# Kernel optimization log

Measured on AMD Instinct MI355X. Metric: run time of the kernel, lower is better.

## Reference

```python
import jax, jax.numpy as jnp
import numpy as np

N_NODES = 10000
N_EDGES = 160000
IN_DIM = 512
HID = 128
HEADS = 8
EMB = 256
NEG_SLOPE = 0.2  # PyG GATConv default


def setup_inputs() -> dict:
    key = jax.random.key(0)
    ks = jax.random.split(key, 12)
    x = jax.random.normal(ks[0], (N_NODES, IN_DIM), dtype=jnp.float32)
    edge_index = jax.random.randint(ks[1], (2, N_EDGES), 0, N_NODES, dtype=jnp.int64)
    s1 = 1.0 / np.sqrt(IN_DIM)
    s2 = 1.0 / np.sqrt(HEADS * HID)
    W1 = jax.random.normal(ks[2], (IN_DIM, HEADS * HID), dtype=jnp.float32) * s1
    a_src1 = jax.random.normal(ks[3], (HEADS, HID), dtype=jnp.float32) * s2
    a_dst1 = jax.random.normal(ks[4], (HEADS, HID), dtype=jnp.float32) * s2
    b1 = jnp.zeros((HEADS * HID,), dtype=jnp.float32)
    W2 = jax.random.normal(ks[5], (HEADS * HID, EMB), dtype=jnp.float32) * s2
    a_src2 = jax.random.normal(ks[6], (1, EMB), dtype=jnp.float32) * (1.0 / np.sqrt(EMB))
    a_dst2 = jax.random.normal(ks[7], (1, EMB), dtype=jnp.float32) * (1.0 / np.sqrt(EMB))
    b2 = jnp.zeros((EMB,), dtype=jnp.float32)
    return {"x": x, "edge_index": edge_index, "W1": W1, "a_src1": a_src1,
            "a_dst1": a_dst1, "b1": b1, "W2": W2, "a_src2": a_src2,
            "a_dst2": a_dst2, "b2": b2}


def gat_layer(h_in, src, dst, W, a_src, a_dst, b, concat, num_nodes):
    """PyG-style GATConv (eval mode, self-loops already in src/dst)."""
    H, C = a_src.shape
    h = (h_in @ W).reshape(num_nodes, H, C)            # [N, H, C]
    alpha_src = jnp.einsum('nhc,hc->nh', h, a_src)      # [N, H]
    alpha_dst = jnp.einsum('nhc,hc->nh', h, a_dst)      # [N, H]
    e = jax.nn.leaky_relu(alpha_src[src] + alpha_dst[dst], NEG_SLOPE)  # [E, H]
    # segment softmax over incoming edges of each destination node
    m = jax.ops.segment_max(e, dst, num_segments=num_nodes)            # [N, H]
    ex = jnp.exp(e - m[dst])
    denom = jax.ops.segment_sum(ex, dst, num_segments=num_nodes)       # [N, H]
    alpha = ex / denom[dst]                                            # [E, H]
    out = jax.ops.segment_sum(h[src] * alpha[:, :, None], dst,
                              num_segments=num_nodes)                  # [N, H, C]
    out = out.reshape(num_nodes, H * C) if concat else out.mean(axis=1)
    return out + b


def reference(x, edge_index, W1, a_src1, a_dst1, b1, W2, a_src2, a_dst2, b2):
    N = x.shape[0]
    loops = jnp.arange(N, dtype=edge_index.dtype)
    src = jnp.concatenate([edge_index[0], loops])
    dst = jnp.concatenate([edge_index[1], loops])
    h = gat_layer(x, src, dst, W1, a_src1, a_dst1, b1, concat=True, num_nodes=N)
    h = jax.nn.elu(h)  # dropout inactive in eval mode
    out = gat_layer(h, src, dst, W2, a_src2, a_dst2, b2, concat=False, num_nodes=N)
    return out
```

## Files before the change

### kernel.cpp

```cpp
#include <hip/hip_runtime.h>
#include <hip/hip_bf16.h>

typedef __attribute__((ext_vector_type(8))) short short8;
typedef __attribute__((ext_vector_type(4))) float floatx4;
typedef __attribute__((ext_vector_type(4))) unsigned short ushort4v;
typedef __attribute__((ext_vector_type(8))) unsigned short ushort8v;
typedef __attribute__((ext_vector_type(2))) unsigned int uint2v;
typedef __attribute__((ext_vector_type(4))) unsigned int uint4v;

#define NN 10000
#define E0 160000
#define ETOT (E0 + NN)
#define IN_DIM 512
#define HID1 1024
#define EMB 256
#define MPAD 10112
#define NX (NN * IN_DIM)
#define NW1 (IN_DIM * HID1)
#define NW2 (HID1 * EMB)

__device__ __forceinline__ float bf2f(unsigned short u) {
    unsigned v = ((unsigned)u) << 16;
    float f;
    __builtin_memcpy(&f, &v, 4);
    return f;
}
__device__ __forceinline__ float bflo(unsigned v) {
    unsigned x = v << 16;
    float f; __builtin_memcpy(&f, &x, 4);
    return f;
}
__device__ __forceinline__ float bfhi(unsigned v) {
    unsigned x = v & 0xffff0000u;
    float f; __builtin_memcpy(&f, &x, 4);
    return f;
}
__device__ __forceinline__ unsigned short f2bf(float f) {
    unsigned u;
    __builtin_memcpy(&u, &f, 4);
    unsigned lsb = (u >> 16) & 1;
    u += 0x7fff + lsb;
    return (unsigned short)(u >> 16);
}
__device__ __forceinline__ float loadf(const void* p, size_t i, int isf32) {
    if (isf32) return ((const float*)p)[i];
    return bf2f(((const unsigned short*)p)[i]);
}
__device__ __forceinline__ float lrelu(float e) { return e > 0.f ? e : 0.2f * e; }

__global__ __launch_bounds__(256) void probezero_kernel(
    const int* __restrict__ ei32, const unsigned* __restrict__ xw,
    int* __restrict__ zbase, int zn, int* __restrict__ eflag, int* __restrict__ isf32)
{
    int b = blockIdx.x, t = threadIdx.x;
    int i = b * 256 + t;
    if (i < zn) zbase[i] = 0;
    if (b == 0) {
        int any = 0;
        #pragma unroll
        for (int k = 0; k < 64; ++k) {
            int idx = (t + k * 256) * 2 + 1;
            any |= ei32[idx];
        }
        __shared__ int sf;
        if (t == 0) sf = 0;
        __syncthreads();
        if (any) atomicOr(&sf, 1);
        __syncthreads();
        if (t == 0) *eflag = sf;
    } else if (b == 1) {
        __shared__ int cnt[256];
        int c = 0;
        #pragma unroll
        for (int j = 0; j < 16; ++j) {
            unsigned w = xw[t * 16 + j];
            int ex = (w >> 7) & 0xFF;
            if (ex >= 110 && ex <= 135) c++;
        }
        cnt[t] = c;
        __syncthreads();
        for (int off = 128; off > 0; off >>= 1) {
            if (t < off) cnt[t] += cnt[t + off];
            __syncthreads();
        }
        if (t == 0) *isf32 = (cnt[0] < 2048) ? 1 : 0;
    }
}

__device__ __forceinline__ int load_edge(const void* ei, long long idx, int m32) {
    if (m32) return ((const int*)ei)[idx];
    return (int)(((const long long*)ei)[idx]);
}

__global__ void count_kernel(const void* ei, const int* flag, int* counts) {
    int e = blockIdx.x * 256 + threadIdx.x;
    if (e < E0) {
        int m32 = (*flag != 0);
        int d = load_edge(ei, (long long)E0 + e, m32);
        if (d >= 0 && d < NN) atomicAdd(&counts[d], 1);
    }
}

__global__ __launch_bounds__(1024) void scan_kernel(const int* counts, int* offsets, int* cursor) {
    __shared__ int wsum[16];
    int t = threadIdx.x;
    int lane = t & 63, wv = t >> 6;
    int base = t * 10;
    int local[10];
    int s = 0;
    #pragma unroll
    for (int j = 0; j < 10; ++j) {
        int idx = base + j;
        int v = (idx < NN) ? (counts[idx] + 1) : 0;
        local[j] = v; s += v;
    }
    int v = s;
    #pragma unroll
    for (int d = 1; d < 64; d <<= 1) {
        int o = __shfl_up(v, d, 64);
        if (lane >= d) v += o;
    }
    if (lane == 63) wsum[wv] = v;
    __syncthreads();
    if (t < 16) {
        int w = wsum[t];
        #pragma unroll
        for (int d = 1; d < 16; d <<= 1) {
            int o = __shfl_up(w, d, 16);
            if (t >= d) w += o;
        }
        wsum[t] = w;
    }
    __syncthreads();
    int woff = (wv == 0) ? 0 : wsum[wv - 1];
    int run = woff + v - s;
    #pragma unroll
    for (int j = 0; j < 10; ++j) {
        int idx = base + j;
        if (idx < NN) { offsets[idx] = run; cursor[idx] = run; run += local[j]; }
    }
    if (t == 1023) offsets[NN] = wsum[15];
}

__global__ void scatter_kernel(const void* ei, const int* flag, int* cursor, int* csr_src) {
    int e = blockIdx.x * 256 + threadIdx.x;
    if (e >= ETOT) return;
    int m32 = (*flag != 0);
    int s, d;
    if (e < E0) { s = load_edge(ei, e, m32); d = load_edge(ei, (long long)E0 + e, m32); }
    else { s = d = e - E0; }
    if (s < 0) s = 0; if (s >= NN) s = NN - 1;
    if (d < 0) d = 0; if (d >= NN) d = NN - 1;
    int pos = atomicAdd(&cursor[d], 1);
    if (pos >= 0 && pos < ETOT) csr_src[pos] = s;
}

__global__ void convall_kernel(const void* x, const void* W1, const void* W2,
                               unsigned short* xb, unsigned short* W1t, unsigned short* W2t,
                               const int* isf32)
{
    int i = blockIdx.x * 256 + threadIdx.x;
    int f = *isf32;
    if (i < NX) { xb[i] = f2bf(loadf(x, i, f)); return; }
    i -= NX;
    if (i < NW1) {
        int r = i / HID1, c = i % HID1;
        W1t[(size_t)c * IN_DIM + r] = f2bf(loadf(W1, i, f));
        return;
    }
    i -= NW1;
    if (i < NW2) {
        int r = i / EMB, c = i % EMB;
        W2t[(size_t)c * HID1 + r] = f2bf(loadf(W2, i, f));
    }
}

template<int HSHIFT, int HN>
__global__ __launch_bounds__(256) void gemm_tile(
    const unsigned short* __restrict__ A,
    const unsigned short* __restrict__ Bt,
    void* __restrict__ Cv, int N, int K,
    const void* __restrict__ a_src, const void* __restrict__ a_dst,
    const int* __restrict__ isf32,
    float* __restrict__ as_out, float* __restrict__ ad_out)
{
    __shared__ unsigned short As[128 * 32];
    __shared__ unsigned short Bs[128 * 32];
    int t = threadIdx.x;
    int wave = t >> 6;
    int lane = t & 63;
    int quad = lane >> 4;
    int l16  = lane & 15;
    int mq = wave & 1, nq = wave >> 1;
    size_t mblk = (size_t)blockIdx.x * 128;
    size_t nblk = (size_t)blockIdx.y * 128;

    floatx4 acc[4][4];
    #pragma unroll
    for (int i = 0; i < 4; ++i)
        #pragma unroll
        for (int j = 0; j < 4; ++j)
            acc[i][j] = (floatx4){0.f, 0.f, 0.f, 0.f};

    const unsigned short* Abase = A + mblk * K;
    const unsigned short* Bbase = Bt + nblk * K;

    for (int kk = 0; kk < K; kk += 32) {
        __syncthreads();
        #pragma unroll
        for (int j = 0; j < 2; ++j) {
            int chunk = (wave << 7) + (j << 6) + lane;
            int r  = chunk >> 2;
            int cs = (chunk & 3) ^ (r & 3);
            const unsigned short* ga = Abase + (size_t)r * K + kk + cs * 8;
            const unsigned short* gb = Bbase + (size_t)r * K + kk + cs * 8;
            __builtin_amdgcn_global_load_lds(
                (const __attribute__((address_space(1))) void*)ga,
                (__attribute__((address_space(3))) void*)(As + (size_t)((wave << 7) + (j << 6)) * 8),
                16, 0, 0);
            __builtin_amdgcn_global_load_lds(
                (const __attribute__((address_space(1))) void*)gb,
                (__attribute__((address_space(3))) void*)(Bs + (size_t)((wave << 7) + (j << 6)) * 8),
                16, 0, 0);
        }
        __syncthreads();

        short8 af[4], bf[4];
        #pragma unroll
        for (int i = 0; i < 4; ++i) {
            int ar = mq * 64 + i * 16 + l16;
            int br = nq * 64 + i * 16 + l16;
            af[i] = *(const short8*)(const void*)(As + ar * 32 + (quad ^ (ar & 3)) * 8);
            bf[i] = *(const short8*)(const void*)(Bs + br * 32 + (quad ^ (br & 3)) * 8);
        }
        #pragma unroll
        for (int i = 0; i < 4; ++i)
            #pragma unroll
            for (int j = 0; j < 4; ++j)
                acc[i][j] = __builtin_amdgcn_mfma_f32_16x16x32_bf16(af[i], bf[j], acc[i][j], 0, 0, 0);
    }

    size_t crow0 = mblk + mq * 64 + quad * 4;
    size_t ccol0 = nblk + nq * 64 + l16;
    #pragma unroll
    for (int i = 0; i < 4; ++i) {
        #pragma unroll
        for (int r = 0; r < 4; ++r) {
            size_t row = crow0 + i * 16 + r;
            size_t b = row * N + ccol0;
            #pragma unroll
            for (int j = 0; j < 4; ++j)
                ((unsigned short*)Cv)[b + j * 16] = f2bf(acc[i][j][r]);
        }
    }

    int f = *isf32;
    float a_s[4], a_d[4];
    #pragma unroll
    for (int j = 0; j < 4; ++j) {
        a_s[j] = loadf(a_src, ccol0 + j * 16, f);
        a_d[j] = loadf(a_dst, ccol0 + j * 16, f);
    }
    int head = (int)((nblk + (size_t)nq * 64) >> HSHIFT);
    #pragma unroll
    for (int i = 0; i < 4; ++i) {
        #pragma unroll
        for (int r = 0; r < 4; ++r) {
            float ps = acc[i][0][r] * a_s[0] + acc[i][1][r] * a_s[1]
                     + acc[i][2][r] * a_s[2] + acc[i][3][r] * a_s[3];
            float pd = acc[i][0][r] * a_d[0] + acc[i][1][r] * a_d[1]
                     + acc[i][2][r] * a_d[2] + acc[i][3][r] * a_d[3];
            #pragma unroll
            for (int off = 1; off < 16; off <<= 1) {
                ps += __shfl_xor(ps, off, 16);
                pd += __shfl_xor(pd, off, 16);
            }
            if (l16 == 0) {
                size_t row = crow0 + i * 16 + r;
                if (row < NN) {
                    atomicAdd(&as_out[row * HN + head], ps);
                    atomicAdd(&ad_out[row * HN + head], pd);
                }
            }
        }
    }
}

__global__ __launch_bounds__(256) void agg1_kernel(
    const unsigned short* __restrict__ h1, const int* __restrict__ offsets,
    const int* __restrict__ csr_src, const float* __restrict__ as1,
    const float* __restrict__ ad1, const void* __restrict__ b1,
    const int* __restrict__ isf32,
    unsigned short* __restrict__ hmid)
{
    int n = blockIdx.x, t = threadIdx.x;
    int f = *isf32;
    int beg = offsets[n], end = offsets[n + 1];
    if (beg < 0) beg = 0; if (end > ETOT) end = ETOT;
    int g = t >> 7;
    int u = t & 127;
    int c0 = u * 8;
    int hc = u >> 4;
    float ad = ad1[n * 8 + hc];

    float den = 0.f;
    float acc[8];
    #pragma unroll
    for (int j = 0; j < 8; ++j) acc[j] = 0.f;

    int i = beg + g;
    for (; i + 6 < end; i += 8) {
        int s0 = csr_src[i];     s0 &= 0x7fffffff; if (s0 >= NN) s0 = 0;
        int s1 = csr_src[i + 2]; s1 &= 0x7fffffff; if (s1 >= NN) s1 = 0;
        int s2 = csr_src[i + 4]; s2 &= 0x7fffffff; if (s2 >= NN) s2 = 0;
        int s3 = csr_src[i + 6]; s3 &= 0x7fffffff; if (s3 >= NN) s3 = 0;
        ushort8v hv0 = *(const ushort8v*)(const void*)(h1 + (size_t)s0 * HID1 + c0);
        ushort8v hv1 = *(const ushort8v*)(const void*)(h1 + (size_t)s1 * HID1 + c0);
        ushort8v hv2 = *(const ushort8v*)(const void*)(h1 + (size_t)s2 * HID1 + c0);
        ushort8v hv3 = *(const ushort8v*)(const void*)(h1 + (size_t)s3 * HID1 + c0);
        float e0 = as1[s0 * 8 + hc] + ad;
        float e1 = as1[s1 * 8 + hc] + ad;
        float e2 = as1[s2 * 8 + hc] + ad;
        float e3 = as1[s3 * 8 + hc] + ad;
        e0 = e0 > 0.f ? e0 : 0.2f * e0;
        e1 = e1 > 0.f ? e1 : 0.2f * e1;
        e2 = e2 > 0.f ? e2 : 0.2f * e2;
        e3 = e3 > 0.f ? e3 : 0.2f * e3;
        float w0 = __expf(e0), w1 = __expf(e1), w2 = __expf(e2), w3 = __expf(e3);
        den += (w0 + w1) + (w2 + w3);
        #pragma unroll
        for (int j = 0; j < 8; ++j)
            acc[j] += (bf2f(hv0[j]) * w0 + bf2f(hv1[j]) * w1)
                    + (bf2f(hv2[j]) * w2 + bf2f(hv3[j]) * w3);
    }
    for (; i + 2 < end; i += 4) {
        int s0 = csr_src[i];     s0 &= 0x7fffffff; if (s0 >= NN) s0 = 0;
        int s1 = csr_src[i + 2]; s1 &= 0x7fffffff; if (s1 >= NN) s1 = 0;
        ushort8v hv0 = *(const ushort8v*)(const void*)(h1 + (size_t)s0 * HID1 + c0);
        ushort8v hv1 = *(const ushort8v*)(const void*)(h1 + (size_t)s1 * HID1 + c0);
        float e0 = as1[s0 * 8 + hc] + ad;
        float e1 = as1[s1 * 8 + hc] + ad;
        e0 = e0 > 0.f ? e0 : 0.2f * e0;
        e1 = e1 > 0.f ? e1 : 0.2f * e1;
        float w0 = __expf(e0), w1 = __expf(e1);
        den += w0 + w1;
        #pragma unroll
        for (int j = 0; j < 8; ++j)
            acc[j] += bf2f(hv0[j]) * w0 + bf2f(hv1[j]) * w1;
    }
    if (i < end) {
        int s0 = csr_src[i]; s0 &= 0x7fffffff; if (s0 >= NN) s0 = 0;
        ushort8v hv0 = *(const ushort8v*)(const void*)(h1 + (size_t)s0 * HID1 + c0);
        float e0 = as1[s0 * 8 + hc] + ad;
        e0 = e0 > 0.f ? e0 : 0.2f * e0;
        float w0 = __expf(e0);
        den += w0;
        #pragma unroll
        for (int j = 0; j < 8; ++j) acc[j] += bf2f(hv0[j]) * w0;
    }

    __shared__ float accsh[128][9];
    __shared__ float densh[128];
    if (g == 1) {
        #pragma unroll
        for (int j = 0; j < 8; ++j) accsh[u][j] = acc[j];
        densh[u] = den;
    }
    __syncthreads();
    if (g == 0) {
        den += densh[u];
        float rden = 1.0f / fmaxf(den, 1e-30f);
        ushort8v outw;
        #pragma unroll
        for (int j = 0; j < 8; ++j) {
            float v = (acc[j] + accsh[u][j]) * rden + loadf(b1, c0 + j, f);
            v = v > 0.f ? v : (__expf(v) - 1.0f);
            outw[j] = f2bf(v);
        }
        *(ushort8v*)(void*)(hmid + (size_t)n * HID1 + c0) = outw;
    }
}

__global__ __launch_bounds__(256) void agg2_kernel(
    const unsigned short* __restrict__ h2, const int* __restrict__ offsets,
    const int* __restrict__ csr_src, const float* __restrict__ as2,
    const float* __restrict__ ad2, const void* __restrict__ b2,
    const int* __restrict__ isf32,
    float* __restrict__ out)
{
    int chunk = blockIdx.x & 3;
    int ng    = blockIdx.x >> 2;
    int n     = ng * 4 + (threadIdx.x >> 6);
    if (n >= NN) return;
    int lane = threadIdx.x & 63;
    int q    = lane >> 4;
    int sl   = lane & 15;
    int f = *isf32;
    int beg = offsets[n], end = offsets[n + 1];
    if (beg < 0) beg = 0; if (end > ETOT) end = ETOT;
    float adn = ad2[n];
    const unsigned* rb = (const unsigned*)h2 + chunk * 32 + sl * 2;

    float den = 0.f;
    float acc[4];
    #pragma unroll
    for (int j = 0; j < 4; ++j) acc[j] = 0.f;

    int i = beg + q;
    for (; i + 12 < end; i += 16) {
        int s0 = csr_src[i];      s0 &= 0x7fffffff; if (s0 >= NN) s0 = 0;
        int s1 = csr_src[i + 4];  s1 &= 0x7fffffff; if (s1 >= NN) s1 = 0;
        int s2 = csr_src[i + 8];  s2 &= 0x7fffffff; if (s2 >= NN) s2 = 0;
        int s3 = csr_src[i + 12]; s3 &= 0x7fffffff; if (s3 >= NN) s3 = 0;
        uint2v v0 = *(const uint2v*)(const void*)(rb + (size_t)s0 * 128);
        uint2v v1 = *(const uint2v*)(const void*)(rb + (size_t)s1 * 128);
        uint2v v2 = *(const uint2v*)(const void*)(rb + (size_t)s2 * 128);
        uint2v v3 = *(const uint2v*)(const void*)(rb + (size_t)s3 * 128);
        float w0 = __expf(lrelu(as2[s0] + adn));
        float w1 = __expf(lrelu(as2[s1] + adn));
        float w2 = __expf(lrelu(as2[s2] + adn));
        float w3 = __expf(lrelu(as2[s3] + adn));
        den += (w0 + w1) + (w2 + w3);
        acc[0] += (bflo(v0[0]) * w0 + bflo(v1[0]) * w1) + (bflo(v2[0]) * w2 + bflo(v3[0]) * w3);
        acc[1] += (bfhi(v0[0]) * w0 + bfhi(v1[0]) * w1) + (bfhi(v2[0]) * w2 + bfhi(v3[0]) * w3);
        acc[2] += (bflo(v0[1]) * w0 + bflo(v1[1]) * w1) + (bflo(v2[1]) * w2 + bflo(v3[1]) * w3);
        acc[3] += (bfhi(v0[1]) * w0 + bfhi(v1[1]) * w1) + (bfhi(v2[1]) * w2 + bfhi(v3[1]) * w3);
    }
    for (; i + 4 < end; i += 8) {
        int s0 = csr_src[i];     s0 &= 0x7fffffff; if (s0 >= NN) s0 = 0;
        int s1 = csr_src[i + 4]; s1 &= 0x7fffffff; if (s1 >= NN) s1 = 0;
        uint2v v0 = *(const uint2v*)(const void*)(rb + (size_t)s0 * 128);
        uint2v v1 = *(const uint2v*)(const void*)(rb + (size_t)s1 * 128);
        float w0 = __expf(lrelu(as2[s0] + adn));
        float w1 = __expf(lrelu(as2[s1] + adn));
        den += w0 + w1;
        acc[0] += bflo(v0[0]) * w0 + bflo(v1[0]) * w1;
        acc[1] += bfhi(v0[0]) * w0 + bfhi(v1[0]) * w1;
        acc[2] += bflo(v0[1]) * w0 + bflo(v1[1]) * w1;
        acc[3] += bfhi(v0[1]) * w0 + bfhi(v1[1]) * w1;
    }
    if (i < end) {
        int s0 = csr_src[i]; s0 &= 0x7fffffff; if (s0 >= NN) s0 = 0;
        uint2v v0 = *(const uint2v*)(const void*)(rb + (size_t)s0 * 128);
        float w0 = __expf(lrelu(as2[s0] + adn));
        den += w0;
        acc[0] += bflo(v0[0]) * w0;
        acc[1] += bfhi(v0[0]) * w0;
        acc[2] += bflo(v0[1]) * w0;
        acc[3] += bfhi(v0[1]) * w0;
    }

    #pragma unroll
    for (int j = 0; j < 4; ++j) {
        acc[j] += __shfl_xor(acc[j], 16, 64);
        acc[j] += __shfl_xor(acc[j], 32, 64);
    }
    den += __shfl_xor(den, 16, 64);
    den += __shfl_xor(den, 32, 64);

    if (q == 0) {
        float rden = 1.0f / fmaxf(den, 1e-30f);
        int c0 = chunk * 64 + sl * 4;
        floatx4 o;
        #pragma unroll
        for (int j = 0; j < 4; ++j)
            o[j] = acc[j] * rden + loadf(b2, c0 + j, f);
        *(floatx4*)(void*)(out + (size_t)n * EMB + c0) = o;
    }
}

extern "C" void kernel_launch(void* const* d_in, const int* in_sizes, int n_in,
                              void* d_out, int out_size, void* d_ws, size_t ws_size,
                              hipStream_t stream)
{
    const void* x      = d_in[0];
    const void* edge   = d_in[1];
    const void* W1     = d_in[2];
    const void* a_src1 = d_in[3];
    const void* a_dst1 = d_in[4];
    const void* b1     = d_in[5];
    const void* W2     = d_in[6];
    const void* a_src2 = d_in[7];
    const void* a_dst2 = d_in[8];
    const void* b2     = d_in[9];
    float* out = (float*)d_out;

    char* ws = (char*)d_ws;
    size_t off = 0;
    auto alloc = [&](size_t bytes) -> void* {
        void* p = ws + off;
        off += (bytes + 255) & ~(size_t)255;
        return p;
    };
    int*            counts = (int*)alloc((size_t)NN * 4);
    float*          as1    = (float*)alloc((size_t)NN * 8 * 4);
    float*          ad1    = (float*)alloc((size_t)NN * 8 * 4);
    float*          as2    = (float*)alloc((size_t)NN * 4);
    float*          ad2    = (float*)alloc((size_t)NN * 4);
    int             zn     = (int)(((char*)ad2 - (char*)counts) / 4) + NN;
    int*            flags  = (int*)alloc(2 * 4);
    int*            offs   = (int*)alloc((NN + 1) * 4);
    int*            cursor = (int*)alloc(NN * 4);
    int*            csr    = (int*)alloc((size_t)ETOT * 4);
    unsigned short* xb     = (unsigned short*)alloc((size_t)MPAD * IN_DIM * 2);
    unsigned short* W1t    = (unsigned short*)alloc((size_t)IN_DIM * HID1 * 2);
    unsigned short* W2t    = (unsigned short*)alloc((size_t)HID1 * EMB * 2);
    unsigned short* h1b    = (unsigned short*)alloc((size_t)MPAD * HID1 * 2);
    unsigned short* hmid   = (unsigned short*)alloc((size_t)MPAD * HID1 * 2);
    unsigned short* h2b    = (unsigned short*)alloc((size_t)MPAD * EMB * 2);
    int* eflag = flags;
    int* isf32 = flags + 1;

    probezero_kernel<<<(zn + 255) / 256, 256, 0, stream>>>(
        (const int*)edge, (const unsigned*)x, counts, zn, eflag, isf32);

    count_kernel<<<(E0 + 255) / 256, 256, 0, stream>>>(edge, eflag, counts);
    scan_kernel<<<1, 1024, 0, stream>>>(counts, offs, cursor);
    scatter_kernel<<<(ETOT + 255) / 256, 256, 0, stream>>>(edge, eflag, cursor, csr);

    convall_kernel<<<(NX + NW1 + NW2 + 255) / 256, 256, 0, stream>>>(
        x, W1, W2, xb, W1t, W2t, isf32);

    dim3 g1(MPAD / 128, HID1 / 128);
    gemm_tile<7, 8><<<g1, 256, 0, stream>>>(xb, W1t, h1b, HID1, IN_DIM,
                                            a_src1, a_dst1, isf32, as1, ad1);

    agg1_kernel<<<NN, 256, 0, stream>>>(h1b, offs, csr, as1, ad1, b1, isf32, hmid);

    dim3 g2(MPAD / 128, EMB / 128);
    gemm_tile<8, 1><<<g2, 256, 0, stream>>>(hmid, W2t, h2b, EMB, HID1,
                                            a_src2, a_dst2, isf32, as2, ad2);

    agg2_kernel<<<(NN / 4) * 4, 256, 0, stream>>>(h2b, offs, csr, as2, ad2, b2, isf32, out);
}
```

Before: 264.6 us.

## Remap agg1 to per-head wavefronts with shuffle reduction instead of shared memory

The layer-1 aggregation kernel now gives each wavefront one (node, head) pair, with each block covering 4 nodes and one head, instead of one block per node covering all 1024 channels. Each lane loads 4 bf16 values (8 bytes) per edge rather than 16 bytes, and the two half-wave partial sums are combined with a cross-lane shuffle instead of a shared-memory exchange and __syncthreads. The aim is to remove the block-level synchronization and shared-memory traffic and to spread gather work more evenly across the GPU. The cost is that CSR indices and attention scores are reloaded once per head, and each per-lane load is narrower.

```diff
diff --git a/kernel.cpp b/kernel.cpp
--- a/kernel.cpp
+++ b/kernel.cpp
@@ -41,6 +41,9 @@
     unsigned lsb = (u >> 16) & 1;
     u += 0x7fff + lsb;
     return (unsigned short)(u >> 16);
+}
+__device__ __forceinline__ unsigned packbf(float lo, float hi) {
+    return (unsigned)f2bf(lo) | ((unsigned)f2bf(hi) << 16);
 }
 __device__ __forceinline__ float loadf(const void* p, size_t i, int isf32) {
     if (isf32) return ((const float*)p)[i];
@@ -293,91 +296,88 @@
     const int* __restrict__ isf32,
     unsigned short* __restrict__ hmid)
 {
-    int n = blockIdx.x, t = threadIdx.x;
+    int head = blockIdx.x & 7;
+    int ng   = blockIdx.x >> 3;
+    int n    = ng * 4 + (threadIdx.x >> 6);
+    if (n >= NN) return;
+    int lane = threadIdx.x & 63;
+    int half = lane >> 5;
+    int sl   = lane & 31;
     int f = *isf32;
     int beg = offsets[n], end = offsets[n + 1];
     if (beg < 0) beg = 0; if (end > ETOT) end = ETOT;
-    int g = t >> 7;
-    int u = t & 127;
-    int c0 = u * 8;
-    int hc = u >> 4;
-    float ad = ad1[n * 8 + hc];
+    float ad = ad1[n * 8 + head];
+    const unsigned* rb = (const unsigned*)h1 + head * 64 + sl * 2;
+    const float* asb = as1 + head;
 
     float den = 0.f;
-    float acc[8];
-    #pragma unroll
-    for (int j = 0; j < 8; ++j) acc[j] = 0.f;
-
-    int i = beg + g;
+    float acc[4];
+    #pragma unroll
+    for (int j = 0; j < 4; ++j) acc[j] = 0.f;
+
+    int i = beg + half;
     for (; i + 6 < end; i += 8) {
         int s0 = csr_src[i];     s0 &= 0x7fffffff; if (s0 >= NN) s0 = 0;
         int s1 = csr_src[i + 2]; s1 &= 0x7fffffff; if (s1 >= NN) s1 = 0;
         int s2 = csr_src[i + 4]; s2 &= 0x7fffffff; if (s2 >= NN) s2 = 0;
         int s3 = csr_src[i + 6]; s3 &= 0x7fffffff; if (s3 >= NN) s3 = 0;
-        ushort8v hv0 = *(const ushort8v*)(const void*)(h1 + (size_t)s0 * HID1 + c0);
-        ushort8v hv1 = *(const ushort8v*)(const void*)(h1 + (size_t)s1 * HID1 + c0);
-        ushort8v hv2 = *(const ushort8v*)(const void*)(h1 + (size_t)s2 * HID1 + c0);
-        ushort8v hv3 = *(const ushort8v*)(const void*)(h1 + (size_t)s3 * HID1 + c0);
-        float e0 = as1[s0 * 8 + hc] + ad;
-        float e1 = as1[s1 * 8 + hc] + ad;
-        float e2 = as1[s2 * 8 + hc] + ad;
-        float e3 = as1[s3 * 8 + hc] + ad;
-        e0 = e0 > 0.f ? e0 : 0.2f * e0;
-        e1 = e1 > 0.f ? e1 : 0.2f * e1;
-        e2 = e2 > 0.f ? e2 : 0.2f * e2;
-        e3 = e3 > 0.f ? e3 : 0.2f * e3;
-        float w0 = __expf(e0), w1 = __expf(e1), w2 = __expf(e2), w3 = __expf(e3);
+        uint2v v0 = *(const uint2v*)(const void*)(rb + (size_t)s0 * 512);
+        uint2v v1 = *(const uint2v*)(const void*)(rb + (size_t)s1 * 512);
+        uint2v v2 = *(const uint2v*)(const void*)(rb + (size_t)s2 * 512);
+        uint2v v3 = *(const uint2v*)(const void*)(rb + (size_t)s3 * 512);
+        float w0 = __expf(lrelu(asb[s0 * 8] + ad));
+        float w1 = __expf(lrelu(asb[s1 * 8] + ad));
+        float w2 = __expf(lrelu(asb[s2 * 8] + ad));
+        float w3 = __expf(lrelu(asb[s3 * 8] + ad));
         den += (w0 + w1) + (w2 + w3);
-        #pragma unroll
-        for (int j = 0; j < 8; ++j)
-            acc[j] += (bf2f(hv0[j]) * w0 + bf2f(hv1[j]) * w1)
-                    + (bf2f(hv2[j]) * w2 + bf2f(hv3[j]) * w3);
+        acc[0] += (bflo(v0[0]) * w0 + bflo(v1[0]) * w1) + (bflo(v2[0]) * w2 + bflo(v3[0]) * w3);
+        acc[1] += (bfhi(v0[0]) * w0 + bfhi(v1[0]) * w1) + (bfhi(v2[0]) * w2 + bfhi(v3[0]) * w3);
+        acc[2] += (bflo(v0[1]) * w0 + bflo(v1[1]) * w1) + (bflo(v2[1]) * w2 + bflo(v3[1]) * w3);
+        acc[3] += (bfhi(v0[1]) * w0 + bfhi(v1[1]) * w1) + (bfhi(v2[1]) * w2 + bfhi(v3[1]) * w3);
     }
     for (; i + 2 < end; i += 4) {
         int s0 = csr_src[i];     s0 &= 0x7fffffff; if (s0 >= NN) s0 = 0;
         int s1 = csr_src[i + 2]; s1 &= 0x7fffffff; if (s1 >= NN) s1 = 0;
-        ushort8v hv0 = *(const ushort8v*)(const void*)(h1 + (size_t)s0 * HID1 + c0);
-        ushort8v hv1 = *(const ushort8v*)(const void*)(h1 + (size_t)s1 * HID1 + c0);
-        float e0 = as1[s0 * 8 + hc] + ad;
-        float e1 = as1[s1 * 8 + hc] + ad;
-        e0 = e0 > 0.f ? e0 : 0.2f * e0;
-        e1 = e1 > 0.f ? e1 : 0.2f * e1;
-        float w0 = __expf(e0), w1 = __expf(e1);
+        uint2v v0 = *(const uint2v*)(const void*)(rb + (size_t)s0 * 512);
+        uint2v v1 = *(const uint2v*)(const void*)(rb + (size_t)s1 * 512);
+        float w0 = __expf(lrelu(asb[s0 * 8] + ad));
+        float w1 = __expf(lrelu(asb[s1 * 8] + ad));
         den += w0 + w1;
-        #pragma unroll
-        for (int j = 0; j < 8; ++j)
-            acc[j] += bf2f(hv0[j]) * w0 + bf2f(hv1[j]) * w1;
+        acc[0] += bflo(v0[0]) * w0 + bflo(v1[0]) * w1;
+        acc[1] += bfhi(v0[0]) * w0 + bfhi(v1[0]) * w1;
+        acc[2] += bflo(v0[1]) * w0 + bflo(v1[1]) * w1;
+        acc[3] += bfhi(v0[1]) * w0 + bfhi(v1[1]) * w1;
     }
     if (i < end) {
         int s0 = csr_src[i]; s0 &= 0x7fffffff; if (s0 >= NN) s0 = 0;
-        ushort8v hv0 = *(const ushort8v*)(const void*)(h1 + (size_t)s0 * HID1 + c0);
-        float e0 = as1[s0 * 8 + hc] + ad;
-        e0 = e0 > 0.f ? e0 : 0.2f * e0;
-        float w0 = __expf(e0);
+        uint2v v0 = *(const uint2v*)(const void*)(rb + (size_t)s0 * 512);
+        float w0 = __expf(lrelu(asb[s0 * 8] + ad));
         den += w0;
-        #pragma unroll
-        for (int j = 0; j < 8; ++j) acc[j] += bf2f(hv0[j]) * w0;
-    }
-
-    __shared__ float accsh[128][9];
-    __shared__ float densh[128];
-    if (g == 1) {
-        #pragma unroll
-        for (int j = 0; j < 8; ++j) accsh[u][j] = acc[j];
-        densh[u] = den;
-    }
-    __syncthreads();
-    if (g == 0) {
-        den += densh[u];
+        acc[0] += bflo(v0[0]) * w0;
+        acc[1] += bfhi(v0[0]) * w0;
+        acc[2] += bflo(v0[1]) * w0;
+        acc[3] += bfhi(v0[1]) * w0;
+    }
+
+    #pragma unroll
+    for (int j = 0; j < 4; ++j) acc[j] += __shfl_xor(acc[j], 32, 64);
+    den += __shfl_xor(den, 32, 64);
+
+    if (half == 0) {
         float rden = 1.0f / fmaxf(den, 1e-30f);
-        ushort8v outw;
-        #pragma unroll
-        for (int j = 0; j < 8; ++j) {
-            float v = (acc[j] + accsh[u][j]) * rden + loadf(b1, c0 + j, f);
-            v = v > 0.f ? v : (__expf(v) - 1.0f);
-            outw[j] = f2bf(v);
-        }
-        *(ushort8v*)(void*)(hmid + (size_t)n * HID1 + c0) = outw;
+        int c0 = head * 128 + sl * 4;
+        float v0 = acc[0] * rden + loadf(b1, c0, f);
+        float v1 = acc[1] * rden + loadf(b1, c0 + 1, f);
+        float v2 = acc[2] * rden + loadf(b1, c0 + 2, f);
+        float v3 = acc[3] * rden + loadf(b1, c0 + 3, f);
+        v0 = v0 > 0.f ? v0 : (__expf(v0) - 1.0f);
+        v1 = v1 > 0.f ? v1 : (__expf(v1) - 1.0f);
+        v2 = v2 > 0.f ? v2 : (__expf(v2) - 1.0f);
+        v3 = v3 > 0.f ? v3 : (__expf(v3) - 1.0f);
+        uint2v o;
+        o[0] = packbf(v0, v1);
+        o[1] = packbf(v2, v3);
+        *(uint2v*)(void*)((unsigned*)hmid + (size_t)n * 512 + head * 64 + sl * 2) = o;
     }
 }
 
@@ -525,7 +525,7 @@
     gemm_tile<7, 8><<<g1, 256, 0, stream>>>(xb, W1t, h1b, HID1, IN_DIM,
                                             a_src1, a_dst1, isf32, as1, ad1);
 
-    agg1_kernel<<<NN, 256, 0, stream>>>(h1b, offs, csr, as1, ad1, b1, isf32, hmid);
+    agg1_kernel<<<(NN / 4) * 8, 256, 0, stream>>>(h1b, offs, csr, as1, ad1, b1, isf32, hmid);
 
     dim3 g2(MPAD / 128, EMB / 128);
     gemm_tile<8, 1><<<g2, 256, 0, stream>>>(hmid, W2t, h2b, EMB, HID1,
```

Result: slower. 271.5 us (+2.6%).

## Split-K the second GEMM with fp32 atomic accumulation and fp32 aggregation input

Applied to the files above, without the earlier changes.

The layer-2 projection GEMM gets a 4-way split-K grid dimension, raising block count from 158 to 632 on a GPU with more compute units than the original grid filled. Partial tiles are accumulated with fp32 atomicAdd into a new fp32 buffer. That buffer is zeroed by the existing zero-init kernel, and agg2 now gathers fp32 rows instead of bf16. In exchange it adds atomic traffic, a larger zeroing pass, and doubles the bytes gathered per edge in the aggregation.

```diff
diff --git a/kernel.cpp b/kernel.cpp
--- a/kernel.cpp
+++ b/kernel.cpp
@@ -175,11 +175,11 @@
     }
 }
 
-template<int HSHIFT, int HN>
+template<int HSHIFT, int HN, bool SPLITK>
 __global__ __launch_bounds__(256) void gemm_tile(
     const unsigned short* __restrict__ A,
     const unsigned short* __restrict__ Bt,
-    void* __restrict__ Cv, int N, int K,
+    void* __restrict__ Cv, int N, int K, int kslice,
     const void* __restrict__ a_src, const void* __restrict__ a_dst,
     const int* __restrict__ isf32,
     float* __restrict__ as_out, float* __restrict__ ad_out)
@@ -194,6 +194,8 @@
     int mq = wave & 1, nq = wave >> 1;
     size_t mblk = (size_t)blockIdx.x * 128;
     size_t nblk = (size_t)blockIdx.y * 128;
+    int kbeg = SPLITK ? blockIdx.z * kslice : 0;
+    int kend = SPLITK ? kbeg + kslice : K;
 
     floatx4 acc[4][4];
     #pragma unroll
@@ -205,7 +207,7 @@
     const unsigned short* Abase = A + mblk * K;
     const unsigned short* Bbase = Bt + nblk * K;
 
-    for (int kk = 0; kk < K; kk += 32) {
+    for (int kk = kbeg; kk < kend; kk += 32) {
         __syncthreads();
         #pragma unroll
         for (int j = 0; j < 2; ++j) {
@@ -249,8 +251,10 @@
             size_t row = crow0 + i * 16 + r;
             size_t b = row * N + ccol0;
             #pragma unroll
-            for (int j = 0; j < 4; ++j)
-                ((unsigned short*)Cv)[b + j * 16] = f2bf(acc[i][j][r]);
+            for (int j = 0; j < 4; ++j) {
+                if (SPLITK) atomicAdd(&((float*)Cv)[b + j * 16], acc[i][j][r]);
+                else        ((unsigned short*)Cv)[b + j * 16] = f2bf(acc[i][j][r]);
+            }
         }
     }
 
@@ -382,7 +386,7 @@
 }
 
 __global__ __launch_bounds__(256) void agg2_kernel(
-    const unsigned short* __restrict__ h2, const int* __restrict__ offsets,
+    const float* __restrict__ h2, const int* __restrict__ offsets,
     const int* __restrict__ csr_src, const float* __restrict__ as2,
     const float* __restrict__ ad2, const void* __restrict__ b2,
     const int* __restrict__ isf32,
@@ -399,7 +403,7 @@
     int beg = offsets[n], end = offsets[n + 1];
     if (beg < 0) beg = 0; if (end > ETOT) end = ETOT;
     float adn = ad2[n];
-    const unsigned* rb = (const unsigned*)h2 + chunk * 32 + sl * 2;
+    const float* rb = h2 + chunk * 64 + sl * 4;
 
     float den = 0.f;
     float acc[4];
@@ -412,42 +416,38 @@
         int s1 = csr_src[i + 4];  s1 &= 0x7fffffff; if (s1 >= NN) s1 = 0;
         int s2 = csr_src[i + 8];  s2 &= 0x7fffffff; if (s2 >= NN) s2 = 0;
         int s3 = csr_src[i + 12]; s3 &= 0x7fffffff; if (s3 >= NN) s3 = 0;
-        uint2v v0 = *(const uint2v*)(const void*)(rb + (size_t)s0 * 128);
-        uint2v v1 = *(const uint2v*)(const void*)(rb + (size_t)s1 * 128);
-        uint2v v2 = *(const uint2v*)(const void*)(rb + (size_t)s2 * 128);
-        uint2v v3 = *(const uint2v*)(const void*)(rb + (size_t)s3 * 128);
+        floatx4 v0 = *(const floatx4*)(const void*)(rb + (size_t)s0 * 256);
+        floatx4 v1 = *(const floatx4*)(const void*)(rb + (size_t)s1 * 256);
+        floatx4 v2 = *(const floatx4*)(const void*)(rb + (size_t)s2 * 256);
+        floatx4 v3 = *(const floatx4*)(const void*)(rb + (size_t)s3 * 256);
         float w0 = __expf(lrelu(as2[s0] + adn));
         float w1 = __expf(lrelu(as2[s1] + adn));
         float w2 = __expf(lrelu(as2[s2] + adn));
         float w3 = __expf(lrelu(as2[s3] + adn));
         den += (w0 + w1) + (w2 + w3);
-        acc[0] += (bflo(v0[0]) * w0 + bflo(v1[0]) * w1) + (bflo(v2[0]) * w2 + bflo(v3[0]) * w3);
-        acc[1] += (bfhi(v0[0]) * w0 + bfhi(v1[0]) * w1) + (bfhi(v2[0]) * w2 + bfhi(v3[0]) * w3);
-        acc[2] += (bflo(v0[1]) * w0 + bflo(v1[1]) * w1) + (bflo(v2[1]) * w2 + bflo(v3[1]) * w3);
-        acc[3] += (bfhi(v0[1]) * w0 + bfhi(v1[1]) * w1) + (bfhi(v2[1]) * w2 + bfhi(v3[1]) * w3);
+        #pragma unroll
+        for (int j = 0; j < 4; ++j)
+            acc[j] += (v0[j] * w0 + v1[j] * w1) + (v2[j] * w2 + v3[j] * w3);
     }
     for (; i + 4 < end; i += 8) {
         int s0 = csr_src[i];     s0 &= 0x7fffffff; if (s0 >= NN) s0 = 0;
         int s1 = csr_src[i + 4]; s1 &= 0x7fffffff; if (s1 >= NN) s1 = 0;
-        uint2v v0 = *(const uint2v*)(const void*)(rb + (size_t)s0 * 128);
-        uint2v v1 = *(const uint2v*)(const void*)(rb + (size_t)s1 * 128);
+        floatx4 v0 = *(const floatx4*)(const void*)(rb + (size_t)s0 * 256);
+        floatx4 v1 = *(const floatx4*)(const void*)(rb + (size_t)s1 * 256);
         float w0 = __expf(lrelu(as2[s0] + adn));
         float w1 = __expf(lrelu(as2[s1] + adn));
         den += w0 + w1;
-        acc[0] += bflo(v0[0]) * w0 + bflo(v1[0]) * w1;
-        acc[1] += bfhi(v0[0]) * w0 + bfhi(v1[0]) * w1;
-        acc[2] += bflo(v0[1]) * w0 + bflo(v1[1]) * w1;
-        acc[3] += bfhi(v0[1]) * w0 + bfhi(v1[1]) * w1;
+        #pragma unroll
+        for (int j = 0; j < 4; ++j)
+            acc[j] += v0[j] * w0 + v1[j] * w1;
     }
     if (i < end) {
         int s0 = csr_src[i]; s0 &= 0x7fffffff; if (s0 >= NN) s0 = 0;
-        uint2v v0 = *(const uint2v*)(const void*)(rb + (size_t)s0 * 128);
+        floatx4 v0 = *(const floatx4*)(const void*)(rb + (size_t)s0 * 256);
         float w0 = __expf(lrelu(as2[s0] + adn));
         den += w0;
-        acc[0] += bflo(v0[0]) * w0;
-        acc[1] += bfhi(v0[0]) * w0;
-        acc[2] += bflo(v0[1]) * w0;
-        acc[3] += bfhi(v0[1]) * w0;
+        #pragma unroll
+        for (int j = 0; j < 4; ++j) acc[j] += v0[j] * w0;
     }
 
     #pragma unroll
@@ -497,7 +497,8 @@
     float*          ad1    = (float*)alloc((size_t)NN * 8 * 4);
     float*          as2    = (float*)alloc((size_t)NN * 4);
     float*          ad2    = (float*)alloc((size_t)NN * 4);
-    int             zn     = (int)(((char*)ad2 - (char*)counts) / 4) + NN;
+    float*          h2f    = (float*)alloc((size_t)MPAD * EMB * 4);
+    int             zn     = (int)(((char*)h2f - (char*)counts) / 4) + MPAD * EMB;
     int*            flags  = (int*)alloc(2 * 4);
     int*            offs   = (int*)alloc((NN + 1) * 4);
     int*            cursor = (int*)alloc(NN * 4);
@@ -507,7 +508,6 @@
     unsigned short* W2t    = (unsigned short*)alloc((size_t)HID1 * EMB * 2);
     unsigned short* h1b    = (unsigned short*)alloc((size_t)MPAD * HID1 * 2);
     unsigned short* hmid   = (unsigned short*)alloc((size_t)MPAD * HID1 * 2);
-    unsigned short* h2b    = (unsigned short*)alloc((size_t)MPAD * EMB * 2);
     int* eflag = flags;
     int* isf32 = flags + 1;
 
@@ -522,14 +522,14 @@
         x, W1, W2, xb, W1t, W2t, isf32);
 
     dim3 g1(MPAD / 128, HID1 / 128);
-    gemm_tile<7, 8><<<g1, 256, 0, stream>>>(xb, W1t, h1b, HID1, IN_DIM,
-                                            a_src1, a_dst1, isf32, as1, ad1);
+    gemm_tile<7, 8, false><<<g1, 256, 0, stream>>>(xb, W1t, h1b, HID1, IN_DIM, 0,
+                                                   a_src1, a_dst1, isf32, as1, ad1);
 
     agg1_kernel<<<NN, 256, 0, stream>>>(h1b, offs, csr, as1, ad1, b1, isf32, hmid);
 
-    dim3 g2(MPAD / 128, EMB / 128);
-    gemm_tile<8, 1><<<g2, 256, 0, stream>>>(hmid, W2t, h2b, EMB, HID1,
-                                            a_src2, a_dst2, isf32, as2, ad2);
-
-    agg2_kernel<<<(NN / 4) * 4, 256, 0, stream>>>(h2b, offs, csr, as2, ad2, b2, isf32, out);
-}
+    dim3 g2(MPAD / 128, EMB / 128, 4);
+    gemm_tile<8, 1, true><<<g2, 256, 0, stream>>>(hmid, W2t, h2f, EMB, HID1, HID1 / 4,
+                                                  a_src2, a_dst2, isf32, as2, ad2);
+
+    agg2_kernel<<<(NN / 4) * 4, 256, 0, stream>>>(h2f, offs, csr, as2, ad2, b2, isf32, out);
+}
```

Measured after the change: 285.5 us. +7.9%, slower.
